# Kernel tuning notes

Hardware: AMD Instinct MI355X
Metric: run time of the kernel (lower is better)

## Reference

```python
import jax, jax.numpy as jnp
import numpy as np
import math

DIM_MODEL = 1024
N_HEAD = 16
NUM_NEURON = 64
MAX_LEN = 2048
B, S = 4, 2048


def setup_inputs() -> dict:
    key = jax.random.key(0)
    ks = jax.random.split(key, 11)
    d, p = DIM_MODEL, N_HEAD * NUM_NEURON
    sc_in = 1.0 / math.sqrt(d)
    sc_p = 1.0 / math.sqrt(p)
    return {
        "q": jax.random.normal(ks[0], (B, S, d), jnp.float32),
        "k": jax.random.normal(ks[1], (B, S, d), jnp.float32),
        "v": jax.random.normal(ks[2], (B, S, d), jnp.float32),
        "Wq": jax.random.normal(ks[3], (d, p), jnp.float32) * sc_in,
        "bq": jnp.zeros((p,), jnp.float32),
        "Wk": jax.random.normal(ks[4], (d, p), jnp.float32) * sc_in,
        "bk": jnp.zeros((p,), jnp.float32),
        "Wv": jax.random.normal(ks[5], (d, p), jnp.float32) * sc_in,
        "bv": jnp.zeros((p,), jnp.float32),
        "Wf": jax.random.normal(ks[6], (p, d), jnp.float32) * sc_p,
        "bf": jnp.zeros((d,), jnp.float32),
    }


def _split_heads(x):  # [B,S,H*Dh] -> [B,H,S,Dh]
    b, s, _ = x.shape
    return x.reshape(b, s, N_HEAD, NUM_NEURON).transpose(0, 2, 1, 3)


def reference(q, k, v, Wq, bq, Wk, bk, Wv, bv, Wf, bf):
    qh = _split_heads(q @ Wq + bq)
    kh = _split_heads(k @ Wk + bk)
    vh = _split_heads(v @ Wv + bv)
    # NOTE: original scales by 1/sqrt(max_len), not 1/sqrt(head_dim)
    scores = jnp.einsum("bhqd,bhkd->bhqk", qh, kh) / math.sqrt(MAX_LEN)
    s = scores.shape[-1]
    causal = jnp.tril(jnp.ones((s, s), bool))  # [S,S]
    scores = jnp.where(causal[None, None], scores, -jnp.inf)
    attn = jax.nn.softmax(scores, axis=-1)
    out = jnp.einsum("bhqk,bhkd->bhqd", attn, vh)  # [B,H,S,Dh]
    c = out.transpose(0, 2, 1, 3).reshape(out.shape[0], out.shape[2], N_HEAD * NUM_NEURON)
    return c @ Wf + bf
```

## Files before the change

### kernel.cpp

```cpp
#include <hip/hip_runtime.h>
#include <stdint.h>

#define DMODEL 1024
#define NHEAD 16
#define DH 64
#define BB 4
#define SS 2048
#define MROWS (BB * SS)

typedef __bf16 bfx8 __attribute__((ext_vector_type(8)));
typedef float f32x4 __attribute__((ext_vector_type(4)));
typedef float fvec4 __attribute__((ext_vector_type(4)));
typedef int i32x4 __attribute__((ext_vector_type(4)));
typedef unsigned short u16x8 __attribute__((ext_vector_type(8)));
typedef unsigned short u16x4 __attribute__((ext_vector_type(4)));

__device__ __forceinline__ unsigned short f2bf(float f) {
    union { float f; unsigned int u; } v; v.f = f;
    unsigned int r = v.u + 0x7FFFu + ((v.u >> 16) & 1u);
    return (unsigned short)(r >> 16);
}

__device__ __forceinline__ unsigned int cvtpk(float lo, float hi) {
    unsigned int r;
    asm("v_cvt_pk_bf16_f32 %0, %1, %2" : "=v"(r) : "v"(lo), "v"(hi));
    return r;
}

typedef __attribute__((address_space(1))) const void gas_t;
typedef __attribute__((address_space(3))) void las_t;
__device__ __forceinline__ void gload_lds16(const void* g, void* l) {
    __builtin_amdgcn_global_load_lds((gas_t*)g, (las_t*)l, 16, 0, 0);
}

__device__ __forceinline__ int sigma_k(int i) {
    return (i & 0x20) | ((i & 0x0C) << 1) | ((i & 0x10) >> 2) | (i & 3);
}

__global__ void cvt3_kernel(const float* __restrict__ s0, const float* __restrict__ s1,
                            const float* __restrict__ s2,
                            unsigned short* __restrict__ d0, unsigned short* __restrict__ d1,
                            unsigned short* __restrict__ d2, int n8)
{
    const float* s = (blockIdx.y == 0) ? s0 : (blockIdx.y == 1) ? s1 : s2;
    unsigned short* d = (blockIdx.y == 0) ? d0 : (blockIdx.y == 1) ? d1 : d2;
    int i = blockIdx.x * blockDim.x + threadIdx.x;
    if (i >= n8) return;
    fvec4 a = *reinterpret_cast<const fvec4*>(&s[(size_t)i * 8]);
    fvec4 b = *reinterpret_cast<const fvec4*>(&s[(size_t)i * 8 + 4]);
    u16x8 o;
    #pragma unroll
    for (int j = 0; j < 4; ++j) { o[j] = f2bf(a[j]); o[j + 4] = f2bf(b[j]); }
    *reinterpret_cast<u16x8*>(&d[(size_t)i * 8]) = o;
}

__global__ void transpose_cvt3_kernel(const float* __restrict__ W0, unsigned short* __restrict__ T0,
                                      const float* __restrict__ W1, unsigned short* __restrict__ T1,
                                      const float* __restrict__ W2, unsigned short* __restrict__ T2)
{
    const float* W = (blockIdx.z == 0) ? W0 : (blockIdx.z == 1) ? W1 : W2;
    unsigned short* Wt = (blockIdx.z == 0) ? T0 : (blockIdx.z == 1) ? T1 : T2;
    __shared__ unsigned short t[64][72];
    const int tid = threadIdx.x;
    const int r0 = blockIdx.y * 64, c0 = blockIdx.x * 64;
    #pragma unroll
    for (int i = 0; i < 4; ++i) {
        int idx = tid + i * 256;
        int r = idx >> 4, c4 = idx & 15;
        fvec4 v = *reinterpret_cast<const fvec4*>(&W[(size_t)(r0 + r) * DMODEL + c0 + c4 * 4]);
        #pragma unroll
        for (int j = 0; j < 4; ++j) t[c4 * 4 + j][r] = f2bf(v[j]);
    }
    __syncthreads();
    #pragma unroll
    for (int i = 0; i < 2; ++i) {
        int idx = tid + i * 256;
        int r = idx >> 3, c8 = idx & 7;
        u16x8 v = *reinterpret_cast<const u16x8*>(&t[r][c8 * 8]);
        *reinterpret_cast<u16x8*>(&Wt[(size_t)(c0 + r) * DMODEL + r0 + c8 * 8]) = v;
    }
}

struct GArg {
    const unsigned short* A;
    const unsigned short* Bt;
    const float* bias;
    void* O;
    float osc;
    int mode;
};

__global__ __launch_bounds__(256, 4)
void gemm_kernel(GArg g0, GArg g1, int M, int N, int K)
{
    const GArg g = blockIdx.z ? g1 : g0;
    __shared__ unsigned short sA[128 * 64];
    __shared__ unsigned short sB[128 * 64];
    const int tid  = threadIdx.x;
    const int lane = tid & 63;
    const int wave = tid >> 6;
    const int wm = (wave >> 1) * 64, wn = (wave & 1) * 64;
    const int m0 = blockIdx.x * 128, n0 = blockIdx.y * 128;
    const int lr = lane & 15;
    const int lg = lane >> 4;

    f32x4 acc[4][4] = {};

    for (int kk0 = 0; kk0 < K; kk0 += 64) {
        __syncthreads();
        #pragma unroll
        for (int i = 0; i < 4; ++i) {
            int c = tid + i * 256;
            int row = c >> 3, col8 = c & 7;
            gload_lds16(&g.A[(size_t)(m0 + row) * K + kk0 + col8 * 8], &sA[c * 8]);
        }
        #pragma unroll
        for (int i = 0; i < 4; ++i) {
            int c = tid + i * 256;
            int row = c >> 3, col8 = c & 7;
            gload_lds16(&g.Bt[(size_t)(n0 + row) * K + kk0 + col8 * 8], &sB[c * 8]);
        }
        __syncthreads();

        #pragma unroll
        for (int kk = 0; kk < 2; ++kk) {
            bfx8 af[4], bfr[4];
            #pragma unroll
            for (int m = 0; m < 4; ++m)
                af[m] = *reinterpret_cast<const bfx8*>(
                    &sA[(wm + m * 16 + lr) * 64 + kk * 32 + lg * 8]);
            #pragma unroll
            for (int n = 0; n < 4; ++n)
                bfr[n] = *reinterpret_cast<const bfx8*>(
                    &sB[(wn + n * 16 + lr) * 64 + kk * 32 + lg * 8]);
            #pragma unroll
            for (int m = 0; m < 4; ++m)
                #pragma unroll
                for (int n = 0; n < 4; ++n)
                    acc[m][n] = __builtin_amdgcn_mfma_f32_16x16x32_bf16(
                        af[m], bfr[n], acc[m][n], 0, 0, 0);
        }
    }

    #pragma unroll
    for (int n = 0; n < 4; ++n) {
        int col = n0 + wn + n * 16 + lr;
        float bv = g.bias[col];
        #pragma unroll
        for (int m = 0; m < 4; ++m) {
            int rowb = m0 + wm + m * 16 + lg * 4;
            float val[4];
            #pragma unroll
            for (int r = 0; r < 4; ++r) val[r] = (acc[m][n][r] + bv) * g.osc;
            if (g.mode == 0) {
                #pragma unroll
                for (int r = 0; r < 4; ++r)
                    ((unsigned short*)g.O)[(size_t)(rowb + r) * N + col] = f2bf(val[r]);
            } else if (g.mode == 2) {
                #pragma unroll
                for (int r = 0; r < 4; ++r)
                    ((float*)g.O)[(size_t)(rowb + r) * N + col] = val[r];
            } else {
                int bq = rowb >> 11, s = rowb & 2047;
                int hh = col >> 6, d = col & 63;
                u16x4 pk;
                #pragma unroll
                for (int r = 0; r < 4; ++r) pk[r] = f2bf(val[r]);
                size_t idx = ((size_t)(bq * 16 + hh) * 64 + d) * 2048 + s;
                *reinterpret_cast<u16x4*>(&((unsigned short*)g.O)[idx]) = pk;
            }
        }
    }
}

__global__ __launch_bounds__(512, 4)
void attn_kernel(const unsigned short* __restrict__ Q,
                 const unsigned short* __restrict__ K,
                 const unsigned short* __restrict__ Vt,
                 unsigned short* __restrict__ C)
{
    __shared__ unsigned short sK[2 * 4096];
    __shared__ unsigned short sV[2 * 4096];

    const int tid  = threadIdx.x;
    const int lane = tid & 63;
    const int wave = tid >> 6;
    const int lr = lane & 15, lg = lane >> 4;
    const int bh = blockIdx.x;
    const int p  = blockIdx.y;
    const int b = bh >> 4, h = bh & 15;
    const size_t rowbase = (size_t)b * SS;
    const int hcol = h * DH;

    const int srow = tid >> 3, sc8 = tid & 7;
    const int sig  = sigma_k(srow);
    const int woff = srow * 64 + ((sc8 ^ (srow & 7)) * 8);
    const int p0 = lg ^ (lr & 7);

    const u16x8 onesu = {0x3F80, 0x3F80, 0x3F80, 0x3F80, 0x3F80, 0x3F80, 0x3F80, 0x3F80};
    union { u16x8 u; bfx8 b; } onesc; onesc.u = onesu;
    const bfx8 ones = onesc.b;

    #pragma unroll
    for (int ph = 0; ph < 2; ++ph) {
        const int qt = ph ? p : (15 - p);
        const int q0 = qt * 128;

        bfx8 aq[2];
        {
            int qr = q0 + wave * 16 + lr;
            const unsigned short* qp = &Q[(rowbase + qr) * DMODEL + hcol + lg * 8];
            aq[0] = *reinterpret_cast<const bfx8*>(qp);
            aq[1] = *reinterpret_cast<const bfx8*>(qp + 32);
        }

        float m_run = 0.f;
        f32x4 acc_l = {};
        f32x4 acc_o[4] = {};
        bool mz = true;
        const int qmax_wave = q0 + wave * 16 + 15;
        const int npairs = qt + 1;

        u16x8 rk[2], rv[2];
        #pragma unroll
        for (int u = 0; u < 2; ++u) {
            rk[u] = *reinterpret_cast<const u16x8*>(
                &K[(rowbase + u * 64 + sig) * DMODEL + hcol + sc8 * 8]);
            rv[u] = *reinterpret_cast<const u16x8*>(
                &Vt[((size_t)bh * DH + srow) * SS + u * 64 + sc8 * 8]);
        }

        for (int u = 0; u < npairs; ++u) {
            __syncthreads();
            #pragma unroll
            for (int s = 0; s < 2; ++s) {
                *reinterpret_cast<u16x8*>(&sK[s * 4096 + woff]) = rk[s];
                *reinterpret_cast<u16x8*>(&sV[s * 4096 + woff]) = rv[s];
            }
            __syncthreads();
            if (u + 1 < npairs) {
                #pragma unroll
                for (int s = 0; s < 2; ++s) {
                    const int kk = (2 * u + 2 + s) * 64;
                    rk[s] = *reinterpret_cast<const u16x8*>(
                        &K[(rowbase + kk + sig) * DMODEL + hcol + sc8 * 8]);
                    rv[s] = *reinterpret_cast<const u16x8*>(
                        &Vt[((size_t)bh * DH + srow) * SS + kk + sc8 * 8]);
                }
            }
            #pragma unroll
            for (int s = 0; s < 2; ++s) {
                const int k0 = (2 * u + s) * 64;
                if (k0 > qmax_wave) break;

                f32x4 sc[4];
                __builtin_amdgcn_s_setprio(1);
                #pragma unroll
                for (int nf = 0; nf < 4; ++nf) {
                    int i = nf * 16 + lr;
                    bfx8 ak0 = *reinterpret_cast<const bfx8*>(&sK[s * 4096 + i * 64 + p0 * 8]);
                    bfx8 ak1 = *reinterpret_cast<const bfx8*>(&sK[s * 4096 + i * 64 + (p0 ^ 4) * 8]);
                    f32x4 sv = {0.f, 0.f, 0.f, 0.f};
                    sv = __builtin_amdgcn_mfma_f32_16x16x32_bf16(ak0, aq[0], sv, 0, 0, 0);
                    sv = __builtin_amdgcn_mfma_f32_16x16x32_bf16(ak1, aq[1], sv, 0, 0, 0);
                    sc[nf] = sv;
                }
                __builtin_amdgcn_s_setprio(0);
                if (k0 + 63 > q0 + wave * 16) {
                    int qrow = q0 + wave * 16 + lr;
                    #pragma unroll
                    for (int nf = 0; nf < 4; ++nf) {
                        int kb = k0 + ((nf >> 1) << 5) + (lg << 3) + ((nf & 1) << 2);
                        #pragma unroll
                        for (int r = 0; r < 4; ++r)
                            if (kb + r > qrow) sc[nf][r] = -3.0e38f;
                    }
                }
                float a0 = fmaxf(fmaxf(sc[0][0], sc[0][1]), sc[0][2]);
                float a1 = fmaxf(fmaxf(sc[0][3], sc[1][0]), sc[1][1]);
                float a2 = fmaxf(fmaxf(sc[1][2], sc[1][3]), sc[2][0]);
                float a3 = fmaxf(fmaxf(sc[2][1], sc[2][2]), sc[2][3]);
                float a4 = fmaxf(fmaxf(sc[3][0], sc[3][1]), sc[3][2]);
                float pmax = fmaxf(fmaxf(fmaxf(a0, a1), fmaxf(a2, a3)),
                                   fmaxf(a4, sc[3][3]));
                if (mz && __all(pmax <= 8.0f)) {
                    #pragma unroll
                    for (int nf = 0; nf < 4; ++nf)
                        #pragma unroll
                        for (int r = 0; r < 4; ++r)
                            sc[nf][r] = __builtin_exp2f(sc[nf][r]);
                } else {
                    mz = false;
                    float mx = pmax;
                    mx = fmaxf(mx, __shfl_xor(mx, 16, 64));
                    mx = fmaxf(mx, __shfl_xor(mx, 32, 64));
                    float mnew = fmaxf(m_run, mx);
                    float fs = __builtin_exp2f(m_run - mnew);
                    m_run = mnew;
                    #pragma unroll
                    for (int nf = 0; nf < 4; ++nf)
                        #pragma unroll
                        for (int r = 0; r < 4; ++r)
                            sc[nf][r] = __builtin_exp2f(sc[nf][r] - mnew);
                    #pragma unroll
                    for (int r = 0; r < 4; ++r) {
                        float fsa = __shfl(fs, lg * 4 + r, 64);
                        #pragma unroll
                        for (int d = 0; d < 4; ++d) acc_o[d][r] *= fsa;
                        acc_l[r] *= fsa;
                    }
                }
                #pragma unroll
                for (int h2 = 0; h2 < 2; ++h2) {
                    union { i32x4 i; bfx8 b; } pa;
                    pa.i[0] = cvtpk(sc[2 * h2][0],     sc[2 * h2][1]);
                    pa.i[1] = cvtpk(sc[2 * h2][2],     sc[2 * h2][3]);
                    pa.i[2] = cvtpk(sc[2 * h2 + 1][0], sc[2 * h2 + 1][1]);
                    pa.i[3] = cvtpk(sc[2 * h2 + 1][2], sc[2 * h2 + 1][3]);
                    __builtin_amdgcn_s_setprio(1);
                    acc_l = __builtin_amdgcn_mfma_f32_16x16x32_bf16(pa.b, ones, acc_l, 0, 0, 0);
                    #pragma unroll
                    for (int d = 0; d < 4; ++d) {
                        int i = d * 16 + lr;
                        int pv = ((h2 << 2) | lg) ^ (lr & 7);
                        bfx8 bv0 = *reinterpret_cast<const bfx8*>(&sV[s * 4096 + i * 64 + pv * 8]);
                        acc_o[d] = __builtin_amdgcn_mfma_f32_16x16x32_bf16(pa.b, bv0, acc_o[d], 0, 0, 0);
                    }
                    __builtin_amdgcn_s_setprio(0);
                }
            }
        }

        f32x4 linv;
        #pragma unroll
        for (int r = 0; r < 4; ++r) linv[r] = 1.0f / acc_l[r];
        const int qrb = q0 + wave * 16 + lg * 4;
        #pragma unroll
        for (int d = 0; d < 4; ++d) {
            int col = hcol + d * 16 + lr;
            #pragma unroll
            for (int r = 0; r < 4; ++r)
                C[(rowbase + qrb + r) * DMODEL + col] = f2bf(acc_o[d][r] * linv[r]);
        }
    }
}

extern "C" void kernel_launch(void* const* d_in, const int* in_sizes, int n_in,
                              void* d_out, int out_size, void* d_ws, size_t ws_size,
                              hipStream_t stream)
{
    const float* q  = (const float*)d_in[0];
    const float* k  = (const float*)d_in[1];
    const float* v  = (const float*)d_in[2];
    const float* Wq = (const float*)d_in[3];
    const float* bq = (const float*)d_in[4];
    const float* Wk = (const float*)d_in[5];
    const float* bk = (const float*)d_in[6];
    const float* Wv = (const float*)d_in[7];
    const float* bv = (const float*)d_in[8];
    const float* Wf = (const float*)d_in[9];
    const float* bf = (const float*)d_in[10];

    unsigned short* ws = (unsigned short*)d_ws;
    const size_t SZ = (size_t)MROWS * DMODEL;
    unsigned short* ws0 = ws;
    unsigned short* ws1 = ws + SZ;
    unsigned short* ws2 = ws + 2 * SZ;
    unsigned short* ws3 = ws + 3 * SZ;

    unsigned short* scr = (unsigned short*)d_out;
    unsigned short* WqT = scr;
    unsigned short* WkT = scr + 1048576;
    unsigned short* WvT = scr + 2097152;
    unsigned short* Qb  = scr + 4194304;

    const float qscale = 0.02209708691207961f * 1.44269504088896341f;

    const int n8 = (int)(SZ / 8);
    cvt3_kernel<<<dim3((n8 + 255) / 256, 3), 256, 0, stream>>>(q, k, v, ws0, ws1, ws2, n8);

    transpose_cvt3_kernel<<<dim3(16, 16, 3), 256, 0, stream>>>(Wq, WqT, Wk, WkT, Wv, WvT);

    {
        GArg gq{ws0, WqT, bq, Qb,  qscale, 0};
        GArg gk{ws1, WkT, bk, ws3, 1.0f,   0};
        gemm_kernel<<<dim3(64, 8, 2), 256, 0, stream>>>(gq, gk, MROWS, DMODEL, DMODEL);
    }
    {
        GArg gv{ws2, WvT, bv, ws0, 1.0f, 3};
        gemm_kernel<<<dim3(64, 8, 1), 256, 0, stream>>>(gv, gv, MROWS, DMODEL, DMODEL);
    }
    transpose_cvt3_kernel<<<dim3(16, 16, 1), 256, 0, stream>>>(Wf, ws2, Wf, ws2, Wf, ws2);

    attn_kernel<<<dim3(BB * NHEAD, 8), 512, 0, stream>>>(Qb, ws3, ws0, ws1);

    {
        GArg gf{ws1, ws2, bf, (float*)d_out, 1.0f, 2};
        gemm_kernel<<<dim3(64, 8, 1), 256, 0, stream>>>(gf, gf, MROWS, DMODEL, DMODEL);
    }
}
```

Before: 193.5 us.

## Share K/V tiles across both query tiles in attention; use 64-row GEMM tiles

The attention kernel now processes its two query tiles (15-p and p) in a single pass over the K/V sequence. Each staged K/V shared-memory tile serves both query tiles, where before the tiles were loaded twice in two sequential phases. This halves K/V global loads and barriers for the short tile, at the cost of more live registers, since two sets of accumulators are held at once. Separately, the GEMM is templated on the M tile size, and the single-matrix V and output projections use 64-row tiles to launch twice as many blocks and improve occupancy and load balance on the GPU.

```diff
diff --git a/kernel.cpp b/kernel.cpp
--- a/kernel.cpp
+++ b/kernel.cpp
@@ -90,26 +90,28 @@
     int mode;
 };
 
+template<int TM>
 __global__ __launch_bounds__(256, 4)
 void gemm_kernel(GArg g0, GArg g1, int M, int N, int K)
 {
+    constexpr int MF = TM / 32;
     const GArg g = blockIdx.z ? g1 : g0;
-    __shared__ unsigned short sA[128 * 64];
+    __shared__ unsigned short sA[TM * 64];
     __shared__ unsigned short sB[128 * 64];
     const int tid  = threadIdx.x;
     const int lane = tid & 63;
     const int wave = tid >> 6;
-    const int wm = (wave >> 1) * 64, wn = (wave & 1) * 64;
-    const int m0 = blockIdx.x * 128, n0 = blockIdx.y * 128;
+    const int wm = (wave >> 1) * (TM / 2), wn = (wave & 1) * 64;
+    const int m0 = blockIdx.x * TM, n0 = blockIdx.y * 128;
     const int lr = lane & 15;
     const int lg = lane >> 4;
 
-    f32x4 acc[4][4] = {};
+    f32x4 acc[MF][4] = {};
 
     for (int kk0 = 0; kk0 < K; kk0 += 64) {
         __syncthreads();
         #pragma unroll
-        for (int i = 0; i < 4; ++i) {
+        for (int i = 0; i < TM / 32; ++i) {
             int c = tid + i * 256;
             int row = c >> 3, col8 = c & 7;
             gload_lds16(&g.A[(size_t)(m0 + row) * K + kk0 + col8 * 8], &sA[c * 8]);
@@ -124,9 +126,9 @@
 
         #pragma unroll
         for (int kk = 0; kk < 2; ++kk) {
-            bfx8 af[4], bfr[4];
-            #pragma unroll
-            for (int m = 0; m < 4; ++m)
+            bfx8 af[MF], bfr[4];
+            #pragma unroll
+            for (int m = 0; m < MF; ++m)
                 af[m] = *reinterpret_cast<const bfx8*>(
                     &sA[(wm + m * 16 + lr) * 64 + kk * 32 + lg * 8]);
             #pragma unroll
@@ -134,7 +136,7 @@
                 bfr[n] = *reinterpret_cast<const bfx8*>(
                     &sB[(wn + n * 16 + lr) * 64 + kk * 32 + lg * 8]);
             #pragma unroll
-            for (int m = 0; m < 4; ++m)
+            for (int m = 0; m < MF; ++m)
                 #pragma unroll
                 for (int n = 0; n < 4; ++n)
                     acc[m][n] = __builtin_amdgcn_mfma_f32_16x16x32_bf16(
@@ -147,7 +149,7 @@
         int col = n0 + wn + n * 16 + lr;
         float bv = g.bias[col];
         #pragma unroll
-        for (int m = 0; m < 4; ++m) {
+        for (int m = 0; m < MF; ++m) {
             int rowb = m0 + wm + m * 16 + lg * 4;
             float val[4];
             #pragma unroll
@@ -188,6 +190,8 @@
     const int lr = lane & 15, lg = lane >> 4;
     const int bh = blockIdx.x;
     const int p  = blockIdx.y;
+    const int qtA = 15 - p, qtB = p;
+    const int q0A = qtA * 128, q0B = qtB * 128;
     const int b = bh >> 4, h = bh & 15;
     const size_t rowbase = (size_t)b * SS;
     const int hcol = h * DH;
@@ -201,136 +205,146 @@
     union { u16x8 u; bfx8 b; } onesc; onesc.u = onesu;
     const bfx8 ones = onesc.b;
 
+    bfx8 aqA[2], aqB[2];
+    {
+        int qrA = q0A + wave * 16 + lr;
+        const unsigned short* qp = &Q[(rowbase + qrA) * DMODEL + hcol + lg * 8];
+        aqA[0] = *reinterpret_cast<const bfx8*>(qp);
+        aqA[1] = *reinterpret_cast<const bfx8*>(qp + 32);
+        int qrB = q0B + wave * 16 + lr;
+        const unsigned short* qb = &Q[(rowbase + qrB) * DMODEL + hcol + lg * 8];
+        aqB[0] = *reinterpret_cast<const bfx8*>(qb);
+        aqB[1] = *reinterpret_cast<const bfx8*>(qb + 32);
+    }
+
+    float m_runA = 0.f, m_runB = 0.f;
+    f32x4 acc_lA = {}, acc_lB = {};
+    f32x4 acc_oA[4] = {}, acc_oB[4] = {};
+    bool mzA = true, mzB = true;
+    const int qmaxA = q0A + wave * 16 + 15;
+    const int qmaxB = q0B + wave * 16 + 15;
+    const int npairs = qtA + 1;
+
+    auto compute = [&](int k0, int q0, bfx8 (&aq)[2], f32x4 (&acc_o)[4],
+                       f32x4& acc_l, float& m_run, bool& mz,
+                       const unsigned short* kb, const unsigned short* vb) {
+        f32x4 sc[4];
+        __builtin_amdgcn_s_setprio(1);
+        #pragma unroll
+        for (int nf = 0; nf < 4; ++nf) {
+            int i = nf * 16 + lr;
+            bfx8 ak0 = *reinterpret_cast<const bfx8*>(&kb[i * 64 + p0 * 8]);
+            bfx8 ak1 = *reinterpret_cast<const bfx8*>(&kb[i * 64 + (p0 ^ 4) * 8]);
+            f32x4 sv = {0.f, 0.f, 0.f, 0.f};
+            sv = __builtin_amdgcn_mfma_f32_16x16x32_bf16(ak0, aq[0], sv, 0, 0, 0);
+            sv = __builtin_amdgcn_mfma_f32_16x16x32_bf16(ak1, aq[1], sv, 0, 0, 0);
+            sc[nf] = sv;
+        }
+        __builtin_amdgcn_s_setprio(0);
+        if (k0 + 63 > q0 + wave * 16) {
+            int qrow = q0 + wave * 16 + lr;
+            #pragma unroll
+            for (int nf = 0; nf < 4; ++nf) {
+                int kb_ = k0 + ((nf >> 1) << 5) + (lg << 3) + ((nf & 1) << 2);
+                #pragma unroll
+                for (int r = 0; r < 4; ++r)
+                    if (kb_ + r > qrow) sc[nf][r] = -3.0e38f;
+            }
+        }
+        float a0 = fmaxf(fmaxf(sc[0][0], sc[0][1]), sc[0][2]);
+        float a1 = fmaxf(fmaxf(sc[0][3], sc[1][0]), sc[1][1]);
+        float a2 = fmaxf(fmaxf(sc[1][2], sc[1][3]), sc[2][0]);
+        float a3 = fmaxf(fmaxf(sc[2][1], sc[2][2]), sc[2][3]);
+        float a4 = fmaxf(fmaxf(sc[3][0], sc[3][1]), sc[3][2]);
+        float pmax = fmaxf(fmaxf(fmaxf(a0, a1), fmaxf(a2, a3)),
+                           fmaxf(a4, sc[3][3]));
+        if (mz && __all(pmax <= 8.0f)) {
+            #pragma unroll
+            for (int nf = 0; nf < 4; ++nf)
+                #pragma unroll
+                for (int r = 0; r < 4; ++r)
+                    sc[nf][r] = __builtin_exp2f(sc[nf][r]);
+        } else {
+            mz = false;
+            float mx = pmax;
+            mx = fmaxf(mx, __shfl_xor(mx, 16, 64));
+            mx = fmaxf(mx, __shfl_xor(mx, 32, 64));
+            float mnew = fmaxf(m_run, mx);
+            float fs = __builtin_exp2f(m_run - mnew);
+            m_run = mnew;
+            #pragma unroll
+            for (int nf = 0; nf < 4; ++nf)
+                #pragma unroll
+                for (int r = 0; r < 4; ++r)
+                    sc[nf][r] = __builtin_exp2f(sc[nf][r] - mnew);
+            #pragma unroll
+            for (int r = 0; r < 4; ++r) {
+                float fsa = __shfl(fs, lg * 4 + r, 64);
+                #pragma unroll
+                for (int d = 0; d < 4; ++d) acc_o[d][r] *= fsa;
+                acc_l[r] *= fsa;
+            }
+        }
+        #pragma unroll
+        for (int h2 = 0; h2 < 2; ++h2) {
+            union { i32x4 i; bfx8 b; } pa;
+            pa.i[0] = cvtpk(sc[2 * h2][0],     sc[2 * h2][1]);
+            pa.i[1] = cvtpk(sc[2 * h2][2],     sc[2 * h2][3]);
+            pa.i[2] = cvtpk(sc[2 * h2 + 1][0], sc[2 * h2 + 1][1]);
+            pa.i[3] = cvtpk(sc[2 * h2 + 1][2], sc[2 * h2 + 1][3]);
+            __builtin_amdgcn_s_setprio(1);
+            acc_l = __builtin_amdgcn_mfma_f32_16x16x32_bf16(pa.b, ones, acc_l, 0, 0, 0);
+            #pragma unroll
+            for (int d = 0; d < 4; ++d) {
+                int i = d * 16 + lr;
+                int pv = ((h2 << 2) | lg) ^ (lr & 7);
+                bfx8 bv0 = *reinterpret_cast<const bfx8*>(&vb[i * 64 + pv * 8]);
+                acc_o[d] = __builtin_amdgcn_mfma_f32_16x16x32_bf16(pa.b, bv0, acc_o[d], 0, 0, 0);
+            }
+            __builtin_amdgcn_s_setprio(0);
+        }
+    };
+
+    u16x8 rk[2], rv[2];
     #pragma unroll
-    for (int ph = 0; ph < 2; ++ph) {
-        const int qt = ph ? p : (15 - p);
-        const int q0 = qt * 128;
-
-        bfx8 aq[2];
-        {
-            int qr = q0 + wave * 16 + lr;
-            const unsigned short* qp = &Q[(rowbase + qr) * DMODEL + hcol + lg * 8];
-            aq[0] = *reinterpret_cast<const bfx8*>(qp);
-            aq[1] = *reinterpret_cast<const bfx8*>(qp + 32);
-        }
-
-        float m_run = 0.f;
-        f32x4 acc_l = {};
-        f32x4 acc_o[4] = {};
-        bool mz = true;
-        const int qmax_wave = q0 + wave * 16 + 15;
-        const int npairs = qt + 1;
-
-        u16x8 rk[2], rv[2];
-        #pragma unroll
-        for (int u = 0; u < 2; ++u) {
-            rk[u] = *reinterpret_cast<const u16x8*>(
-                &K[(rowbase + u * 64 + sig) * DMODEL + hcol + sc8 * 8]);
-            rv[u] = *reinterpret_cast<const u16x8*>(
-                &Vt[((size_t)bh * DH + srow) * SS + u * 64 + sc8 * 8]);
-        }
-
-        for (int u = 0; u < npairs; ++u) {
-            __syncthreads();
+    for (int s = 0; s < 2; ++s) {
+        rk[s] = *reinterpret_cast<const u16x8*>(
+            &K[(rowbase + s * 64 + sig) * DMODEL + hcol + sc8 * 8]);
+        rv[s] = *reinterpret_cast<const u16x8*>(
+            &Vt[((size_t)bh * DH + srow) * SS + s * 64 + sc8 * 8]);
+    }
+
+    for (int u = 0; u < npairs; ++u) {
+        __syncthreads();
+        #pragma unroll
+        for (int s = 0; s < 2; ++s) {
+            *reinterpret_cast<u16x8*>(&sK[s * 4096 + woff]) = rk[s];
+            *reinterpret_cast<u16x8*>(&sV[s * 4096 + woff]) = rv[s];
+        }
+        __syncthreads();
+        if (u + 1 < npairs) {
             #pragma unroll
             for (int s = 0; s < 2; ++s) {
-                *reinterpret_cast<u16x8*>(&sK[s * 4096 + woff]) = rk[s];
-                *reinterpret_cast<u16x8*>(&sV[s * 4096 + woff]) = rv[s];
+                const int kk = (2 * u + 2 + s) * 64;
+                rk[s] = *reinterpret_cast<const u16x8*>(
+                    &K[(rowbase + kk + sig) * DMODEL + hcol + sc8 * 8]);
+                rv[s] = *reinterpret_cast<const u16x8*>(
+                    &Vt[((size_t)bh * DH + srow) * SS + kk + sc8 * 8]);
             }
-            __syncthreads();
-            if (u + 1 < npairs) {
-                #pragma unroll
-                for (int s = 0; s < 2; ++s) {
-                    const int kk = (2 * u + 2 + s) * 64;
-                    rk[s] = *reinterpret_cast<const u16x8*>(
-                        &K[(rowbase + kk + sig) * DMODEL + hcol + sc8 * 8]);
-                    rv[s] = *reinterpret_cast<const u16x8*>(
-                        &Vt[((size_t)bh * DH + srow) * SS + kk + sc8 * 8]);
-                }
-            }
-            #pragma unroll
-            for (int s = 0; s < 2; ++s) {
-                const int k0 = (2 * u + s) * 64;
-                if (k0 > qmax_wave) break;
-
-                f32x4 sc[4];
-                __builtin_amdgcn_s_setprio(1);
-                #pragma unroll
-                for (int nf = 0; nf < 4; ++nf) {
-                    int i = nf * 16 + lr;
-                    bfx8 ak0 = *reinterpret_cast<const bfx8*>(&sK[s * 4096 + i * 64 + p0 * 8]);
-                    bfx8 ak1 = *reinterpret_cast<const bfx8*>(&sK[s * 4096 + i * 64 + (p0 ^ 4) * 8]);
-                    f32x4 sv = {0.f, 0.f, 0.f, 0.f};
-                    sv = __builtin_amdgcn_mfma_f32_16x16x32_bf16(ak0, aq[0], sv, 0, 0, 0);
-                    sv = __builtin_amdgcn_mfma_f32_16x16x32_bf16(ak1, aq[1], sv, 0, 0, 0);
-                    sc[nf] = sv;
-                }
-                __builtin_amdgcn_s_setprio(0);
-                if (k0 + 63 > q0 + wave * 16) {
-                    int qrow = q0 + wave * 16 + lr;
-                    #pragma unroll
-                    for (int nf = 0; nf < 4; ++nf) {
-                        int kb = k0 + ((nf >> 1) << 5) + (lg << 3) + ((nf & 1) << 2);
-                        #pragma unroll
-                        for (int r = 0; r < 4; ++r)
-                            if (kb + r > qrow) sc[nf][r] = -3.0e38f;
-                    }
-                }
-                float a0 = fmaxf(fmaxf(sc[0][0], sc[0][1]), sc[0][2]);
-                float a1 = fmaxf(fmaxf(sc[0][3], sc[1][0]), sc[1][1]);
-                float a2 = fmaxf(fmaxf(sc[1][2], sc[1][3]), sc[2][0]);
-                float a3 = fmaxf(fmaxf(sc[2][1], sc[2][2]), sc[2][3]);
-                float a4 = fmaxf(fmaxf(sc[3][0], sc[3][1]), sc[3][2]);
-                float pmax = fmaxf(fmaxf(fmaxf(a0, a1), fmaxf(a2, a3)),
-                                   fmaxf(a4, sc[3][3]));
-                if (mz && __all(pmax <= 8.0f)) {
-                    #pragma unroll
-                    for (int nf = 0; nf < 4; ++nf)
-                        #pragma unroll
-                        for (int r = 0; r < 4; ++r)
-                            sc[nf][r] = __builtin_exp2f(sc[nf][r]);
-                } else {
-                    mz = false;
-                    float mx = pmax;
-                    mx = fmaxf(mx, __shfl_xor(mx, 16, 64));
-                    mx = fmaxf(mx, __shfl_xor(mx, 32, 64));
-                    float mnew = fmaxf(m_run, mx);
-                    float fs = __builtin_exp2f(m_run - mnew);
-                    m_run = mnew;
-                    #pragma unroll
-                    for (int nf = 0; nf < 4; ++nf)
-                        #pragma unroll
-                        for (int r = 0; r < 4; ++r)
-                            sc[nf][r] = __builtin_exp2f(sc[nf][r] - mnew);
-                    #pragma unroll
-                    for (int r = 0; r < 4; ++r) {
-                        float fsa = __shfl(fs, lg * 4 + r, 64);
-                        #pragma unroll
-                        for (int d = 0; d < 4; ++d) acc_o[d][r] *= fsa;
-                        acc_l[r] *= fsa;
-                    }
-                }
-                #pragma unroll
-                for (int h2 = 0; h2 < 2; ++h2) {
-                    union { i32x4 i; bfx8 b; } pa;
-                    pa.i[0] = cvtpk(sc[2 * h2][0],     sc[2 * h2][1]);
-                    pa.i[1] = cvtpk(sc[2 * h2][2],     sc[2 * h2][3]);
-                    pa.i[2] = cvtpk(sc[2 * h2 + 1][0], sc[2 * h2 + 1][1]);
-                    pa.i[3] = cvtpk(sc[2 * h2 + 1][2], sc[2 * h2 + 1][3]);
-                    __builtin_amdgcn_s_setprio(1);
-                    acc_l = __builtin_amdgcn_mfma_f32_16x16x32_bf16(pa.b, ones, acc_l, 0, 0, 0);
-                    #pragma unroll
-                    for (int d = 0; d < 4; ++d) {
-                        int i = d * 16 + lr;
-                        int pv = ((h2 << 2) | lg) ^ (lr & 7);
-                        bfx8 bv0 = *reinterpret_cast<const bfx8*>(&sV[s * 4096 + i * 64 + pv * 8]);
-                        acc_o[d] = __builtin_amdgcn_mfma_f32_16x16x32_bf16(pa.b, bv0, acc_o[d], 0, 0, 0);
-                    }
-                    __builtin_amdgcn_s_setprio(0);
-                }
-            }
-        }
-
+        }
+        #pragma unroll
+        for (int s = 0; s < 2; ++s) {
+            const int k0 = (2 * u + s) * 64;
+            const unsigned short* kb = &sK[s * 4096];
+            const unsigned short* vb = &sV[s * 4096];
+            if (k0 <= qmaxA)
+                compute(k0, q0A, aqA, acc_oA, acc_lA, m_runA, mzA, kb, vb);
+            if (k0 <= qmaxB)
+                compute(k0, q0B, aqB, acc_oB, acc_lB, m_runB, mzB, kb, vb);
+        }
+    }
+
+    auto epi = [&](int q0, f32x4 (&acc_o)[4], f32x4& acc_l) {
         f32x4 linv;
         #pragma unroll
         for (int r = 0; r < 4; ++r) linv[r] = 1.0f / acc_l[r];
@@ -342,7 +356,9 @@
             for (int r = 0; r < 4; ++r)
                 C[(rowbase + qrb + r) * DMODEL + col] = f2bf(acc_o[d][r] * linv[r]);
         }
-    }
+    };
+    epi(q0A, acc_oA, acc_lA);
+    epi(q0B, acc_oB, acc_lB);
 }
 
 extern "C" void kernel_launch(void* const* d_in, const int* in_sizes, int n_in,
@@ -384,11 +400,11 @@
     {
         GArg gq{ws0, WqT, bq, Qb,  qscale, 0};
         GArg gk{ws1, WkT, bk, ws3, 1.0f,   0};
-        gemm_kernel<<<dim3(64, 8, 2), 256, 0, stream>>>(gq, gk, MROWS, DMODEL, DMODEL);
+        gemm_kernel<128><<<dim3(64, 8, 2), 256, 0, stream>>>(gq, gk, MROWS, DMODEL, DMODEL);
     }
     {
         GArg gv{ws2, WvT, bv, ws0, 1.0f, 3};
-        gemm_kernel<<<dim3(64, 8, 1), 256, 0, stream>>>(gv, gv, MROWS, DMODEL, DMODEL);
+        gemm_kernel<64><<<dim3(128, 8, 1), 256, 0, stream>>>(gv, gv, MROWS, DMODEL, DMODEL);
     }
     transpose_cvt3_kernel<<<dim3(16, 16, 1), 256, 0, stream>>>(Wf, ws2, Wf, ws2, Wf, ws2);
 
@@ -396,6 +412,6 @@
 
     {
         GArg gf{ws1, ws2, bf, (float*)d_out, 1.0f, 2};
-        gemm_kernel<<<dim3(64, 8, 1), 256, 0, stream>>>(gf, gf, MROWS, DMODEL, DMODEL);
-    }
-}
+        gemm_kernel<64><<<dim3(128, 8, 1), 256, 0, stream>>>(gf, gf, MROWS, DMODEL, DMODEL);
+    }
+}
```

Result: slower. 248.5 us (+28.4%).

## Double-buffer K/V shared memory tiles to halve barriers per iteration

Applied to the files above, without the earlier changes.

Shared memory for K and V tiles becomes two ping-pong buffers. Each iteration computes on the current buffer, then stores the prefetched registers into the other buffer and issues the next global loads, with one barrier per iteration instead of two. This removes a synchronization point and lets the LDS writes for the next tile overlap with other waves' compute. In exchange the LDS footprint doubles to 64KB per block, which may lower occupancy at 512 threads with launch_bounds(512,4).

```diff
diff --git a/kernel.cpp b/kernel.cpp
--- a/kernel.cpp
+++ b/kernel.cpp
@@ -179,8 +179,8 @@
                  const unsigned short* __restrict__ Vt,
                  unsigned short* __restrict__ C)
 {
-    __shared__ unsigned short sK[2 * 4096];
-    __shared__ unsigned short sV[2 * 4096];
+    __shared__ unsigned short sK[2][8192];
+    __shared__ unsigned short sV[2][8192];
 
     const int tid  = threadIdx.x;
     const int lane = tid & 63;
@@ -223,31 +223,31 @@
 
         u16x8 rk[2], rv[2];
         #pragma unroll
-        for (int u = 0; u < 2; ++u) {
-            rk[u] = *reinterpret_cast<const u16x8*>(
-                &K[(rowbase + u * 64 + sig) * DMODEL + hcol + sc8 * 8]);
-            rv[u] = *reinterpret_cast<const u16x8*>(
-                &Vt[((size_t)bh * DH + srow) * SS + u * 64 + sc8 * 8]);
-        }
+        for (int s = 0; s < 2; ++s) {
+            rk[s] = *reinterpret_cast<const u16x8*>(
+                &K[(rowbase + s * 64 + sig) * DMODEL + hcol + sc8 * 8]);
+            rv[s] = *reinterpret_cast<const u16x8*>(
+                &Vt[((size_t)bh * DH + srow) * SS + s * 64 + sc8 * 8]);
+        }
+        #pragma unroll
+        for (int s = 0; s < 2; ++s) {
+            *reinterpret_cast<u16x8*>(&sK[0][s * 4096 + woff]) = rk[s];
+            *reinterpret_cast<u16x8*>(&sV[0][s * 4096 + woff]) = rv[s];
+        }
+        if (npairs > 1) {
+            #pragma unroll
+            for (int s = 0; s < 2; ++s) {
+                const int kk = (2 + s) * 64;
+                rk[s] = *reinterpret_cast<const u16x8*>(
+                    &K[(rowbase + kk + sig) * DMODEL + hcol + sc8 * 8]);
+                rv[s] = *reinterpret_cast<const u16x8*>(
+                    &Vt[((size_t)bh * DH + srow) * SS + kk + sc8 * 8]);
+            }
+        }
+        __syncthreads();
 
         for (int u = 0; u < npairs; ++u) {
-            __syncthreads();
-            #pragma unroll
-            for (int s = 0; s < 2; ++s) {
-                *reinterpret_cast<u16x8*>(&sK[s * 4096 + woff]) = rk[s];
-                *reinterpret_cast<u16x8*>(&sV[s * 4096 + woff]) = rv[s];
-            }
-            __syncthreads();
-            if (u + 1 < npairs) {
-                #pragma unroll
-                for (int s = 0; s < 2; ++s) {
-                    const int kk = (2 * u + 2 + s) * 64;
-                    rk[s] = *reinterpret_cast<const u16x8*>(
-                        &K[(rowbase + kk + sig) * DMODEL + hcol + sc8 * 8]);
-                    rv[s] = *reinterpret_cast<const u16x8*>(
-                        &Vt[((size_t)bh * DH + srow) * SS + kk + sc8 * 8]);
-                }
-            }
+            const int cur = u & 1;
             #pragma unroll
             for (int s = 0; s < 2; ++s) {
                 const int k0 = (2 * u + s) * 64;
@@ -258,8 +258,8 @@
                 #pragma unroll
                 for (int nf = 0; nf < 4; ++nf) {
                     int i = nf * 16 + lr;
-                    bfx8 ak0 = *reinterpret_cast<const bfx8*>(&sK[s * 4096 + i * 64 + p0 * 8]);
-                    bfx8 ak1 = *reinterpret_cast<const bfx8*>(&sK[s * 4096 + i * 64 + (p0 ^ 4) * 8]);
+                    bfx8 ak0 = *reinterpret_cast<const bfx8*>(&sK[cur][s * 4096 + i * 64 + p0 * 8]);
+                    bfx8 ak1 = *reinterpret_cast<const bfx8*>(&sK[cur][s * 4096 + i * 64 + (p0 ^ 4) * 8]);
                     f32x4 sv = {0.f, 0.f, 0.f, 0.f};
                     sv = __builtin_amdgcn_mfma_f32_16x16x32_bf16(ak0, aq[0], sv, 0, 0, 0);
                     sv = __builtin_amdgcn_mfma_f32_16x16x32_bf16(ak1, aq[1], sv, 0, 0, 0);
@@ -323,12 +323,30 @@
                     for (int d = 0; d < 4; ++d) {
                         int i = d * 16 + lr;
                         int pv = ((h2 << 2) | lg) ^ (lr & 7);
-                        bfx8 bv0 = *reinterpret_cast<const bfx8*>(&sV[s * 4096 + i * 64 + pv * 8]);
+                        bfx8 bv0 = *reinterpret_cast<const bfx8*>(&sV[cur][s * 4096 + i * 64 + pv * 8]);
                         acc_o[d] = __builtin_amdgcn_mfma_f32_16x16x32_bf16(pa.b, bv0, acc_o[d], 0, 0, 0);
                     }
                     __builtin_amdgcn_s_setprio(0);
                 }
             }
+            if (u + 1 < npairs) {
+                #pragma unroll
+                for (int s = 0; s < 2; ++s) {
+                    *reinterpret_cast<u16x8*>(&sK[cur ^ 1][s * 4096 + woff]) = rk[s];
+                    *reinterpret_cast<u16x8*>(&sV[cur ^ 1][s * 4096 + woff]) = rv[s];
+                }
+                if (u + 2 < npairs) {
+                    #pragma unroll
+                    for (int s = 0; s < 2; ++s) {
+                        const int kk = (2 * u + 4 + s) * 64;
+                        rk[s] = *reinterpret_cast<const u16x8*>(
+                            &K[(rowbase + kk + sig) * DMODEL + hcol + sc8 * 8]);
+                        rv[s] = *reinterpret_cast<const u16x8*>(
+                            &Vt[((size_t)bh * DH + srow) * SS + kk + sc8 * 8]);
+                    }
+                }
+            }
+            __syncthreads();
         }
 
         f32x4 linv;
```

After: 193.3 us. No clear change (-0.1%).
